# Performance work log

Hardware: AMD Instinct MI355X
Metric: run time of the kernel (lower is better)

Reference implementation:

```python
import jax, jax.numpy as jnp
import numpy as np
from jax import lax

B, N, D_PTS = 8, 4096, 6
N_POINTS, N_SAMPLES, RADIUS = 1024, 32, 0.2
MLPS = [64, 64, 128]
BN_EPS = 1e-3  # keras BatchNormalization default epsilon


def safe_norm(diff, axis):
    # euclidean norm with a backward-safe sqrt (same forward values)
    sq = jnp.sum(diff * diff, axis=axis)
    pos = sq > 0
    return jnp.where(pos, jnp.sqrt(jnp.where(pos, sq, 1.0)), 0.0)


def setup_inputs() -> dict:
    key = jax.random.key(0)
    ks = jax.random.split(key, 2)
    xyz = jax.random.normal(ks[0], (B, N, 3), jnp.float32)
    points = jax.random.normal(ks[1], (B, N, D_PTS), jnp.float32)
    inp = {"xyz": xyz, "points": points}
    c_in = 3 + D_PTS
    for i, c_out in enumerate(MLPS):
        kw = jax.random.fold_in(key, 100 + i)
        inp[f"w{i}"] = jax.random.normal(kw, (c_in, c_out), jnp.float32) * (1.0 / np.sqrt(c_in))
        inp[f"b{i}"] = jnp.zeros((c_out,), jnp.float32)
        inp[f"g{i}"] = jnp.ones((c_out,), jnp.float32)
        inp[f"be{i}"] = jnp.zeros((c_out,), jnp.float32)
        c_in = c_out
    return inp


def fps(xyz, n_points):
    # farthest point sampling; original seeds with a random index, we use 0 deterministically
    b, n, _ = xyz.shape
    init_idx = jnp.zeros((b,), jnp.int32)
    mask0 = jnp.ones((b, n), xyz.dtype)
    def step(carry, _):
        mask, last = carry
        added = jnp.take_along_axis(xyz, last[:, None, None], axis=1)  # [B,1,D]
        dist = safe_norm(xyz - added, 2) * mask                        # [B,N]
        nxt = jnp.argmax(dist, axis=1).astype(jnp.int32)
        new_mask = jnp.minimum(dist * mask * 1e11, mask)
        return (new_mask, nxt), nxt
    _, ids = lax.scan(step, (mask0, init_idx), None, length=n_points - 1)
    return jnp.concatenate([init_idx[:, None], ids.T], axis=1)  # [B, n_points]


def gather_points(x, idx):
    # x: [B,N,C]; idx: [B,...] -> [B,...,C]
    b = x.shape[0]
    flat = idx.reshape(b, -1)
    out = jnp.take_along_axis(x, flat[..., None], axis=1)
    return out.reshape(idx.shape + (x.shape[-1],))


def query_ball(radius, n_samples, xyz, cent_xyz):
    # faithful to source: compares norm to radius**2 (source quirk), full argsort then slice
    diff = xyz[:, None, :, :] - cent_xyz[:, :, None, :]   # [B,n,N,3]
    dist = safe_norm(diff, 3)                              # [B,n,N]
    dist = jnp.minimum(dist, radius * radius)
    return jnp.argsort(dist, axis=2)[:, :, :n_samples]     # [B,n,n_samples]


def mlp_layer(h, w, b, g, be):
    # pointwise Dense + BatchNormalization (batch stats, axis=-1) + relu
    h = jnp.einsum('bnsc,cd->bnsd', h, w) + b
    mean = jnp.mean(h, axis=(0, 1, 2), keepdims=True)
    var = jnp.var(h, axis=(0, 1, 2), keepdims=True)
    h = g * (h - mean) * lax.rsqrt(var + BN_EPS) + be
    return jax.nn.relu(h)


def forward(xyz, points, params):
    cent_idx = fps(xyz, N_POINTS)                 # [B, n_points]
    cent_xyz = gather_points(xyz, cent_idx)       # [B, n_points, 3]
    group_idx = query_ball(RADIUS, N_SAMPLES, xyz, cent_xyz)  # [B, n_points, n_samples]
    group_xyz = gather_points(xyz, group_idx)     # [B, n_points, n_samples, 3]
    group_pts = gather_points(points, group_idx)  # [B, n_points, n_samples, D]
    h = jnp.concatenate([group_xyz, group_pts], axis=-1)
    for (w, b, g, be) in params:
        h = mlp_layer(h, w, b, g, be)
    return cent_xyz, jnp.max(h, axis=2)           # [B,n_points,3], [B,n_points,128]


def reference(xyz, points, w0, b0, g0, be0, w1, b1, g1, be1, w2, b2, g2, be2):
    params = [(w0, b0, g0, be0), (w1, b1, g1, be1), (w2, b2, g2, be2)]
    return forward(xyz, points, params)
```

## Files before the change

kernel.cpp:

```cpp
#include <hip/hip_runtime.h>

#define NPTS  4096
#define NB    8
#define NC    1024
#define NSAMP 32
#define DP    6
#define C0    9
#define C3    128
#define ROWS_TOT 262144

#define OFF_SS   (32ull<<10)
#define OFF_H0   (1ull<<20)
#define OFF_Y0   (16ull<<20)
#define OFF_Y1   (96ull<<20)
#define OFF_PSUM (168ull<<20)
#define OFF_PSQ  (172ull<<20)
#define OFF_GMX  (176ull<<20)
#define OFF_GMN  (180ull<<20)

typedef unsigned long long ull;

__device__ __forceinline__ float sqdist_noc(float x, float y, float z,
                                            float cx, float cy, float cz) {
  #pragma clang fp contract(off)
  float dx = x - cx, dy = y - cy, dz = z - cz;
  return dx * dx + dy * dy + dz * dz;
}

template <int CTRL, int RM>
__device__ __forceinline__ ull dpp_mov_u64(ull x) {
  int lo = (int)(unsigned)(x & 0xFFFFFFFFull);
  int hi = (int)(unsigned)(x >> 32);
  int rlo = __builtin_amdgcn_update_dpp(lo, lo, CTRL, RM, 0xf, false);
  int rhi = __builtin_amdgcn_update_dpp(hi, hi, CTRL, RM, 0xf, false);
  return ((ull)(unsigned)rhi << 32) | (unsigned)rlo;
}

__device__ __forceinline__ ull umax64(ull a, ull b) { return a > b ? a : b; }

__device__ __forceinline__ ull wave64_umax(ull x) {
  x = umax64(x, dpp_mov_u64<0x111, 0xf>(x));
  x = umax64(x, dpp_mov_u64<0x112, 0xf>(x));
  x = umax64(x, dpp_mov_u64<0x114, 0xf>(x));
  x = umax64(x, dpp_mov_u64<0x118, 0xf>(x));
  x = umax64(x, dpp_mov_u64<0x142, 0xa>(x));
  x = umax64(x, dpp_mov_u64<0x143, 0xc>(x));
  return x;
}

__global__ __launch_bounds__(256)
void fps_kernel(const float* __restrict__ xyz, float* __restrict__ cent) {
  const int b = blockIdx.x;
  const int t = threadIdx.x;
  const float* X = xyz + (size_t)b * NPTS * 3;
  float* OC = cent + (size_t)b * NC * 3;

  __shared__ float4 sxyz[NPTS];
  __shared__ alignas(16) ull wk[2][4];
  __shared__ int sidx[NC];

  for (int p = t; p < NPTS; p += 256)
    sxyz[p] = make_float4(X[p * 3 + 0], X[p * 3 + 1], X[p * 3 + 2], 0.f);
  __syncthreads();

  float px[16], py[16], pz[16], h[16];
  #pragma unroll
  for (int i = 0; i < 16; i++) {
    float4 v = sxyz[t * 16 + i];
    px[i] = v.x; py[i] = v.y; pz[i] = v.z;
    h[i] = fmaf(v.x, v.x, fmaf(v.y, v.y, v.z * v.z));
  }

  int last = 0;
  for (int k = 1; k < NC; k++) {
    const int par = k & 1;
    if (t == 0) sidx[k - 1] = last;
    float4 c = sxyz[last];
    const float cx2 = -2.0f * c.x, cy2 = -2.0f * c.y, cz2 = -2.0f * c.z;
    if ((last >> 4) == t) {
      int ii = last & 15;
      #pragma unroll
      for (int i = 0; i < 16; i++)
        if (i == ii) h[i] = -__builtin_inff();
    }

    float mx = -__builtin_inff(); int mj = 0;
    #pragma unroll
    for (int i = 0; i < 16; i++) {
      float key = fmaf(pz[i], cz2, fmaf(py[i], cy2, fmaf(px[i], cx2, h[i])));
      if (key > mx) { mx = key; mj = i; }
    }
    unsigned mb = __float_as_uint(mx);
    mb ^= (unsigned)((int)mb >> 31) | 0x80000000u;
    ull key = ((ull)mb << 12) | (unsigned)(4095 - (t * 16 + mj));
    key = wave64_umax(key);

    if ((t & 63) == 63) wk[par][t >> 6] = key;
    __syncthreads();
    const ulonglong2* W2 = (const ulonglong2*)&wk[par][0];
    ulonglong2 p0 = W2[0], p1 = W2[1];
    last = 4095 - (int)(umax64(umax64(p0.x, p0.y), umax64(p1.x, p1.y)) & 0xFFFull);
  }
  if (t == 0) sidx[NC - 1] = last;
  __syncthreads();
  for (int i = t; i < NC; i += 256) {
    float4 c = sxyz[sidx[i]];
    OC[i * 3 + 0] = c.x;
    OC[i * 3 + 1] = c.y;
    OC[i * 3 + 2] = c.z;
  }
}

#define BCAP 256
__global__ __launch_bounds__(256)
void ball_kernel(const float* __restrict__ xyz, const float* __restrict__ pts,
                 const float* __restrict__ cent, float* __restrict__ h0) {
  const int blk = blockIdx.x;
  const int b = blk >> 10;
  const int t = threadIdx.x;
  const float* X = xyz + (size_t)b * NPTS * 3;
  const float* P = pts + (size_t)b * NPTS * DP;
  const float cx = cent[(size_t)blk * 3 + 0];
  const float cy = cent[(size_t)blk * 3 + 1];
  const float cz = cent[(size_t)blk * 3 + 2];

  __shared__ int scount;
  __shared__ ull skeys[BCAP];
  __shared__ ull ssorted[BCAP];
  __shared__ int sel[NSAMP];
  if (t == 0) scount = 0;
  __syncthreads();

  #pragma unroll
  for (int i = 0; i < 16; i++) {
    int j = t * 16 + i;
    float sq = sqdist_noc(X[j * 3 + 0], X[j * 3 + 1], X[j * 3 + 2], cx, cy, cz);
    if (sq < 0.0017f) {
      float d = (sq > 0.f) ? sqrtf(sq) : 0.f;
      if (d < 0.04f) {
        int pos = atomicAdd(&scount, 1);
        if (pos < BCAP)
          skeys[pos] = ((ull)(unsigned)__float_as_int(d) << 12) | (unsigned)j;
      }
    }
  }
  __syncthreads();
  const int M = min(scount, BCAP);

  if (t < M) {
    ull my = skeys[t];
    int r = 0;
    for (int j2 = 0; j2 < M; j2++) r += (skeys[j2] < my);
    ssorted[r] = my;
  }
  __syncthreads();

  if (t < NSAMP) {
    int v;
    if (t < M) {
      v = (int)(ssorted[t] & 0xFFFull);
    } else {
      int s = t - M;
      int idx = s;
      for (int it = 0; it < 40; it++) {
        int c = 0;
        for (int j2 = 0; j2 < M; j2++) c += ((int)(skeys[j2] & 0xFFFull) <= idx);
        int nidx = s + c;
        if (nidx == idx) break;
        idx = nidx;
      }
      v = idx;
    }
    sel[t] = v;
  }
  __syncthreads();

  float* H = h0 + (size_t)blk * NSAMP * C0;
  for (int e = t; e < NSAMP * C0; e += 256) {
    int k = e / C0;
    int c = e - k * C0;
    int j = sel[k];
    H[e] = (c < 3) ? X[j * 3 + c] : P[j * DP + (c - 3)];
  }
}

__global__ __launch_bounds__(256)
void dense0_kernel(const float* __restrict__ h0, const float* __restrict__ W,
                   const float* __restrict__ bias, float* __restrict__ yout,
                   float* __restrict__ psum, float* __restrict__ psq) {
  __shared__ float xs[64 * C0];
  __shared__ float ws[C0 * 64];
  __shared__ float red[2][16][64];
  const int blk = blockIdx.x, t = threadIdx.x;
  const size_t rbase = (size_t)blk * 64;
  for (int e = t; e < 64 * C0; e += 256) xs[e] = h0[rbase * C0 + e];
  for (int e = t; e < C0 * 64; e += 256) ws[e] = W[e];
  __syncthreads();
  const int rg = t >> 4, cg = t & 15;
  float acc[4][4];
  float4 bv = *(const float4*)(bias + cg * 4);
  #pragma unroll
  for (int r = 0; r < 4; r++) { acc[r][0] = bv.x; acc[r][1] = bv.y; acc[r][2] = bv.z; acc[r][3] = bv.w; }
  #pragma unroll
  for (int k = 0; k < C0; k++) {
    float4 wv = *(const float4*)(ws + k * 64 + cg * 4);
    #pragma unroll
    for (int r = 0; r < 4; r++) {
      float x = xs[(rg * 4 + r) * C0 + k];
      acc[r][0] = fmaf(x, wv.x, acc[r][0]);
      acc[r][1] = fmaf(x, wv.y, acc[r][1]);
      acc[r][2] = fmaf(x, wv.z, acc[r][2]);
      acc[r][3] = fmaf(x, wv.w, acc[r][3]);
    }
  }
  #pragma unroll
  for (int r = 0; r < 4; r++)
    *(float4*)(yout + (rbase + rg * 4 + r) * 64 + cg * 4) =
        make_float4(acc[r][0], acc[r][1], acc[r][2], acc[r][3]);
  #pragma unroll
  for (int c4 = 0; c4 < 4; c4++) {
    float s = 0.f, q = 0.f;
    #pragma unroll
    for (int r = 0; r < 4; r++) { float v = acc[r][c4]; s += v; q = fmaf(v, v, q); }
    red[0][rg][cg * 4 + c4] = s;
    red[1][rg][cg * 4 + c4] = q;
  }
  __syncthreads();
  if (t < 64) {
    float S = 0.f, Q = 0.f;
    #pragma unroll
    for (int g = 0; g < 16; g++) { S += red[0][g][t]; Q += red[1][g][t]; }
    psum[(size_t)t * 4096 + blk] = S;
    psq [(size_t)t * 4096 + blk] = Q;
  }
}

template <int RPB, int COUT, int CGN, int NBLKS, bool MM>
__global__ __launch_bounds__(256)
void dense_mid_kernel(const float* __restrict__ yin, const float* __restrict__ ssin,
                      const float* __restrict__ W, const float* __restrict__ bias,
                      float* __restrict__ yout,
                      float* __restrict__ psum, float* __restrict__ psq,
                      float* __restrict__ gmax, float* __restrict__ gmin) {
  constexpr int NG = 256 / CGN;
  __shared__ float xs[RPB * 68];
  __shared__ float ws[64 * COUT];
  __shared__ float scs[64], shs[64];
  __shared__ float red[2][NG][COUT];
  __shared__ float redm[MM ? 2 : 1][MM ? NG : 1][MM ? COUT : 1];
  const int blk = blockIdx.x, t = threadIdx.x;
  if (t < 64) { scs[t] = ssin[t]; shs[t] = ssin[128 + t]; }
  __syncthreads();
  const size_t rbase = (size_t)blk * RPB;
  for (int e = t; e < RPB * 64; e += 256) {
    int c = e & 63;
    float v = yin[rbase * 64 + e];
    xs[(e >> 6) * 68 + c] = fmaxf(fmaf(v, scs[c], shs[c]), 0.f);
  }
  for (int e = t; e < 64 * COUT; e += 256) ws[e] = W[e];
  __syncthreads();
  const int rg = t / CGN, cg = t % CGN;
  float acc[4][4];
  float4 bv = *(const float4*)(bias + cg * 4);
  #pragma unroll
  for (int r = 0; r < 4; r++) { acc[r][0] = bv.x; acc[r][1] = bv.y; acc[r][2] = bv.z; acc[r][3] = bv.w; }
  for (int k0 = 0; k0 < 64; k0 += 4) {
    float4 xv[4];
    #pragma unroll
    for (int r = 0; r < 4; r++)
      xv[r] = *(const float4*)(xs + (rg * 4 + r) * 68 + k0);
    #pragma unroll
    for (int kk = 0; kk < 4; kk++) {
      float4 wv = *(const float4*)(ws + (k0 + kk) * COUT + cg * 4);
      #pragma unroll
      for (int r = 0; r < 4; r++) {
        float x = (&xv[r].x)[kk];
        acc[r][0] = fmaf(x, wv.x, acc[r][0]);
        acc[r][1] = fmaf(x, wv.y, acc[r][1]);
        acc[r][2] = fmaf(x, wv.z, acc[r][2]);
        acc[r][3] = fmaf(x, wv.w, acc[r][3]);
      }
    }
  }
  if constexpr (!MM) {
    #pragma unroll
    for (int r = 0; r < 4; r++)
      *(float4*)(yout + (rbase + rg * 4 + r) * COUT + cg * 4) =
          make_float4(acc[r][0], acc[r][1], acc[r][2], acc[r][3]);
  }
  #pragma unroll
  for (int c4 = 0; c4 < 4; c4++) {
    float s = 0.f, q = 0.f;
    #pragma unroll
    for (int r = 0; r < 4; r++) { float v = acc[r][c4]; s += v; q = fmaf(v, v, q); }
    red[0][rg][cg * 4 + c4] = s;
    red[1][rg][cg * 4 + c4] = q;
    if constexpr (MM) {
      float mx = acc[0][c4], mn = acc[0][c4];
      #pragma unroll
      for (int r = 1; r < 4; r++) { mx = fmaxf(mx, acc[r][c4]); mn = fminf(mn, acc[r][c4]); }
      redm[0][rg][cg * 4 + c4] = mx;
      redm[1][rg][cg * 4 + c4] = mn;
    }
  }
  __syncthreads();
  if (t < COUT) {
    float S = 0.f, Q = 0.f;
    #pragma unroll
    for (int g = 0; g < NG; g++) { S += red[0][g][t]; Q += red[1][g][t]; }
    psum[(size_t)t * NBLKS + blk] = S;
    psq [(size_t)t * NBLKS + blk] = Q;
    if constexpr (MM) {
      float mx = redm[0][0][t], mn = redm[1][0][t];
      #pragma unroll
      for (int g = 1; g < NG; g++) { mx = fmaxf(mx, redm[0][g][t]); mn = fminf(mn, redm[1][g][t]); }
      gmax[(size_t)blk * COUT + t] = mx;
      gmin[(size_t)blk * COUT + t] = mn;
    }
  }
}

template <int NBLK>
__global__ __launch_bounds__(256)
void stats_final_kernel(const float* __restrict__ psum, const float* __restrict__ psq,
                        const float* __restrict__ g, const float* __restrict__ be,
                        float* __restrict__ ss_out) {
  const int c = blockIdx.x, t = threadIdx.x;
  float S = 0.f, Q = 0.f;
  for (int i = t; i < NBLK; i += 256) {
    S += psum[(size_t)c * NBLK + i];
    Q += psq [(size_t)c * NBLK + i];
  }
  __shared__ float sS[256], sQ[256];
  sS[t] = S; sQ[t] = Q;
  __syncthreads();
  #pragma unroll
  for (int off = 128; off; off >>= 1) {
    if (t < off) { sS[t] += sS[t + off]; sQ[t] += sQ[t + off]; }
    __syncthreads();
  }
  if (t == 0) {
    const float inv = 1.0f / 262144.0f;
    float mean = sS[0] * inv;
    float var = sQ[0] * inv - mean * mean;
    float scale = g[c] / sqrtf(var + 1e-3f);
    ss_out[c] = scale;
    ss_out[128 + c] = be[c] - mean * scale;
  }
}

__global__ __launch_bounds__(128)
void pool_final_kernel(const float* __restrict__ gmax, const float* __restrict__ gmin,
                       const float* __restrict__ ss2, float* __restrict__ out1) {
  const int blk = blockIdx.x, c = threadIdx.x;
  const float sc = ss2[c], sh = ss2[128 + c];
  float v = (sc >= 0.f) ? gmax[(size_t)blk * C3 + c] : gmin[(size_t)blk * C3 + c];
  out1[(size_t)blk * C3 + c] = fmaxf(fmaf(v, sc, sh), 0.f);
}

extern "C" void kernel_launch(void* const* d_in, const int* in_sizes, int n_in,
                              void* d_out, int out_size, void* d_ws, size_t ws_size,
                              hipStream_t stream) {
  const float* xyz = (const float*)d_in[0];
  const float* pts = (const float*)d_in[1];
  const float* w0 = (const float*)d_in[2];
  const float* b0 = (const float*)d_in[3];
  const float* g0 = (const float*)d_in[4];
  const float* be0 = (const float*)d_in[5];
  const float* w1 = (const float*)d_in[6];
  const float* b1 = (const float*)d_in[7];
  const float* g1 = (const float*)d_in[8];
  const float* be1 = (const float*)d_in[9];
  const float* w2 = (const float*)d_in[10];
  const float* b2 = (const float*)d_in[11];
  const float* g2 = (const float*)d_in[12];
  const float* be2 = (const float*)d_in[13];

  float* out = (float*)d_out;
  float* cent = out;
  float* out1 = out + (size_t)NB * NC * 3;

  char* ws = (char*)d_ws;
  float* ssA  = (float*)(ws + OFF_SS);
  float* h0   = (float*)(ws + OFF_H0);
  float* y0   = (float*)(ws + OFF_Y0);
  float* y1   = (float*)(ws + OFF_Y1);
  float* psum = (float*)(ws + OFF_PSUM);
  float* psq  = (float*)(ws + OFF_PSQ);
  float* gmx  = (float*)(ws + OFF_GMX);
  float* gmn  = (float*)(ws + OFF_GMN);

  fps_kernel<<<dim3(NB), dim3(256), 0, stream>>>(xyz, cent);
  ball_kernel<<<dim3(NB * NC), dim3(256), 0, stream>>>(xyz, pts, cent, h0);

  dense0_kernel<<<dim3(ROWS_TOT / 64), dim3(256), 0, stream>>>(h0, w0, b0, y0, psum, psq);
  stats_final_kernel<4096><<<dim3(64), dim3(256), 0, stream>>>(psum, psq, g0, be0, ssA + 0 * 256);

  dense_mid_kernel<64, 64, 16, 4096, false><<<dim3(ROWS_TOT / 64), dim3(256), 0, stream>>>(
      y0, ssA + 0 * 256, w1, b1, y1, psum, psq, nullptr, nullptr);
  stats_final_kernel<4096><<<dim3(64), dim3(256), 0, stream>>>(psum, psq, g1, be1, ssA + 1 * 256);

  dense_mid_kernel<32, 128, 32, 8192, true><<<dim3(ROWS_TOT / 32), dim3(256), 0, stream>>>(
      y1, ssA + 1 * 256, w2, b2, nullptr, psum, psq, gmx, gmn);
  stats_final_kernel<8192><<<dim3(128), dim3(256), 0, stream>>>(psum, psq, g2, be2, ssA + 2 * 256);

  pool_final_kernel<<<dim3(NB * NC), dim3(128), 0, stream>>>(gmx, gmn, ssA + 2 * 256, out1);

  (void)in_sizes; (void)n_in; (void)out_size; (void)ws_size;
}
```

Baseline: 963.3 us.

## Shorten FPS critical path with float wave max and staged candidate coordinates

Replaces the 64-bit packed key wave reduction with a 32-bit float DPP max plus readlane. The winning lane writes its candidate's coordinates and index to shared memory, so the next step reads the centroid directly instead of doing a dependent LDS lookup. The per-thread argmax becomes a tree reduction to cut serial dependency depth. Tie-breaking changes: when lanes hold equal maxima, several may write and the surviving index is not necessarily the lowest, unlike the previous packed key.

```diff
diff --git a/kernel.cpp b/kernel.cpp
--- a/kernel.cpp
+++ b/kernel.cpp
@@ -28,23 +28,19 @@
 }
 
 template <int CTRL, int RM>
-__device__ __forceinline__ ull dpp_mov_u64(ull x) {
-  int lo = (int)(unsigned)(x & 0xFFFFFFFFull);
-  int hi = (int)(unsigned)(x >> 32);
-  int rlo = __builtin_amdgcn_update_dpp(lo, lo, CTRL, RM, 0xf, false);
-  int rhi = __builtin_amdgcn_update_dpp(hi, hi, CTRL, RM, 0xf, false);
-  return ((ull)(unsigned)rhi << 32) | (unsigned)rlo;
-}
-
-__device__ __forceinline__ ull umax64(ull a, ull b) { return a > b ? a : b; }
-
-__device__ __forceinline__ ull wave64_umax(ull x) {
-  x = umax64(x, dpp_mov_u64<0x111, 0xf>(x));
-  x = umax64(x, dpp_mov_u64<0x112, 0xf>(x));
-  x = umax64(x, dpp_mov_u64<0x114, 0xf>(x));
-  x = umax64(x, dpp_mov_u64<0x118, 0xf>(x));
-  x = umax64(x, dpp_mov_u64<0x142, 0xa>(x));
-  x = umax64(x, dpp_mov_u64<0x143, 0xc>(x));
+__device__ __forceinline__ float dpp_mov_f(float x) {
+  int xi = __float_as_int(x);
+  int r = __builtin_amdgcn_update_dpp(xi, xi, CTRL, RM, 0xf, false);
+  return __int_as_float(r);
+}
+
+__device__ __forceinline__ float wave64_fmax(float x) {
+  x = fmaxf(x, dpp_mov_f<0x111, 0xf>(x));
+  x = fmaxf(x, dpp_mov_f<0x112, 0xf>(x));
+  x = fmaxf(x, dpp_mov_f<0x114, 0xf>(x));
+  x = fmaxf(x, dpp_mov_f<0x118, 0xf>(x));
+  x = fmaxf(x, dpp_mov_f<0x142, 0xa>(x));
+  x = fmaxf(x, dpp_mov_f<0x143, 0xc>(x));
   return x;
 }
 
@@ -56,7 +52,8 @@
   float* OC = cent + (size_t)b * NC * 3;
 
   __shared__ float4 sxyz[NPTS];
-  __shared__ alignas(16) ull wk[2][4];
+  __shared__ float4 wkc[2][4];
+  __shared__ alignas(16) int wki[2][4];
   __shared__ int sidx[NC];
 
   for (int p = t; p < NPTS; p += 256)
@@ -71,43 +68,74 @@
     h[i] = fmaf(v.x, v.x, fmaf(v.y, v.y, v.z * v.z));
   }
 
-  int last = 0;
-  for (int k = 1; k < NC; k++) {
-    const int par = k & 1;
-    if (t == 0) sidx[k - 1] = last;
-    float4 c = sxyz[last];
-    const float cx2 = -2.0f * c.x, cy2 = -2.0f * c.y, cz2 = -2.0f * c.z;
-    if ((last >> 4) == t) {
-      int ii = last & 15;
+  const int wv = t >> 6;
+  float4 c;
+
+  auto step_body = [&](int pw_) {
+    const float c2x = c.x + c.x, c2y = c.y + c.y, c2z = c.z + c.z;
+    float key[16]; int idx[16];
+    #pragma unroll
+    for (int i = 0; i < 16; i++) {
+      key[i] = fmaf(pz[i], -c2z, fmaf(py[i], -c2y, fmaf(px[i], -c2x, h[i])));
+      idx[i] = i;
+    }
+    #pragma unroll
+    for (int s = 1; s < 16; s <<= 1) {
+      #pragma unroll
+      for (int i = 0; i < 16; i += 2 * s) {
+        bool tk = key[i + s] > key[i];
+        key[i] = tk ? key[i + s] : key[i];
+        idx[i] = tk ? idx[i + s] : idx[i];
+      }
+    }
+    const float mx = key[0];
+    const int mj = idx[0];
+    float4 cand = sxyz[(t << 4) + mj];
+    float wm = wave64_fmax(mx);
+    float smax = __int_as_float(__builtin_amdgcn_readlane(__float_as_int(wm), 63));
+    if (mx == smax) {
+      wkc[pw_][wv] = make_float4(cand.x, cand.y, cand.z, smax);
+      wki[pw_][wv] = (t << 4) + mj;
+    }
+  };
+
+  auto fold = [&](int pr_) -> int {
+    float4 q0 = wkc[pr_][0], q1 = wkc[pr_][1];
+    float4 q2 = wkc[pr_][2], q3 = wkc[pr_][3];
+    const int4 ii = *(const int4*)&wki[pr_][0];
+    bool g1 = q1.w > q0.w; float4 ca = g1 ? q1 : q0; int ia = g1 ? ii.y : ii.x;
+    bool g3 = q3.w > q2.w; float4 cb = g3 ? q3 : q2; int ib = g3 ? ii.w : ii.z;
+    bool gb = cb.w > ca.w; c = gb ? cb : ca; return gb ? ib : ia;
+  };
+
+  if (t == 0) { sidx[0] = 0; h[0] = -__builtin_inff(); }
+  c = sxyz[0];
+  step_body(1);
+  __syncthreads();
+
+  for (int k = 2; k < NC; k++) {
+    const int pr = (k - 1) & 1, pw = k & 1;
+    int gidx = fold(pr);
+    if (t == 0) sidx[k - 1] = gidx;
+    if ((gidx >> 4) == t) {
+      int m = gidx & 15;
       #pragma unroll
       for (int i = 0; i < 16; i++)
-        if (i == ii) h[i] = -__builtin_inff();
-    }
-
-    float mx = -__builtin_inff(); int mj = 0;
-    #pragma unroll
-    for (int i = 0; i < 16; i++) {
-      float key = fmaf(pz[i], cz2, fmaf(py[i], cy2, fmaf(px[i], cx2, h[i])));
-      if (key > mx) { mx = key; mj = i; }
-    }
-    unsigned mb = __float_as_uint(mx);
-    mb ^= (unsigned)((int)mb >> 31) | 0x80000000u;
-    ull key = ((ull)mb << 12) | (unsigned)(4095 - (t * 16 + mj));
-    key = wave64_umax(key);
-
-    if ((t & 63) == 63) wk[par][t >> 6] = key;
+        if (i == m) h[i] = -__builtin_inff();
+    }
+    step_body(pw);
     __syncthreads();
-    const ulonglong2* W2 = (const ulonglong2*)&wk[par][0];
-    ulonglong2 p0 = W2[0], p1 = W2[1];
-    last = 4095 - (int)(umax64(umax64(p0.x, p0.y), umax64(p1.x, p1.y)) & 0xFFFull);
-  }
-  if (t == 0) sidx[NC - 1] = last;
+  }
+  {
+    int gidx = fold(1023 & 1);
+    if (t == 0) sidx[NC - 1] = gidx;
+  }
   __syncthreads();
   for (int i = t; i < NC; i += 256) {
-    float4 c = sxyz[sidx[i]];
-    OC[i * 3 + 0] = c.x;
-    OC[i * 3 + 1] = c.y;
-    OC[i * 3 + 2] = c.z;
+    float4 cc = sxyz[sidx[i]];
+    OC[i * 3 + 0] = cc.x;
+    OC[i * 3 + 1] = cc.y;
+    OC[i * 3 + 2] = cc.z;
   }
 }
 
```

Result: faster. 885.3 us (-8.1%).
